# Optimization experiments

Measured on AMD Instinct MI355X. Metric: run time of the kernel, lower is better.

The kernel has to match this reference:

```python
import jax, jax.numpy as jnp
import numpy as np

TH = 0.1            # inference_th
PNUM = 20           # positive_num (also Pmax pad width for per-level top-k)
PLAM = 1.0          # positive_lambda
ANCHOR_SIZES = (64.0, 128.0)   # box_coder.anchor_sizes, one per FPN level
N, C = 2, 30
LEVELS = [(100, 136, 8, 64.0), (50, 68, 16, 128.0)]  # (H, W, stride, anchor_size)
NEG = -1e30


def make_anchors(H, W, stride, size):
    ys = (jnp.arange(H, dtype=jnp.float32) + 0.5) * stride
    xs = (jnp.arange(W, dtype=jnp.float32) + 0.5) * stride
    cy, cx = jnp.meshgrid(ys, xs, indexing='ij')
    cx, cy = cx.reshape(-1), cy.reshape(-1)
    h = size / 2.0
    return jnp.stack([cx - h, cy - h, cx + h, cy + h], axis=-1)  # [HW,4] x1y1x2y2


def setup_inputs() -> dict:
    key = jax.random.key(0)
    ks = iter(jax.random.split(key, 64))
    inp = {}
    for h in range(1, 5):
        for li, (H, W, _, _) in enumerate(LEVELS):
            suf = 'ab'[li]
            inp[f'cls{h}{suf}'] = jax.random.normal(next(ks), (N, C, H, W), jnp.float32)
            inp[f'reg{h}{suf}'] = jax.random.normal(next(ks), (N, C * 16, H, W), jnp.float32) * 0.1
    inp['anchors_a'] = make_anchors(*LEVELS[0])
    inp['anchors_b'] = make_anchors(*LEVELS[1])
    return inp


def _level(cls, reg, anchors):
    # permute_and_flatten (A=1) + sigmoid + threshold + dense keypoint decode
    n, c, H, W = cls.shape
    hw = H * W
    s = jax.nn.sigmoid(jnp.transpose(cls.reshape(n, c, hw), (0, 2, 1)))          # [N,HW,C]
    r = jnp.transpose(reg.reshape(n, c * 16, hw), (0, 2, 1)).reshape(n, hw, c, 16)
    x1, y1, x2, y2 = anchors[:, 0], anchors[:, 1], anchors[:, 2], anchors[:, 3]
    wa = (x2 - x1)[None, :, None, None]
    ha = (y2 - y1)[None, :, None, None]
    cxa = ((x1 + x2) * 0.5)[None, :, None, None]
    cya = ((y1 + y2) * 0.5)[None, :, None, None]
    kx = r[..., :8] * wa + cxa                                                    # 8 keypoint x's
    ky = r[..., 8:] * ha + cya                                                    # 8 keypoint y's
    dets = jnp.concatenate([kx, ky], axis=-1)                                     # [N,HW,C,16]
    mask = s > TH
    sm = jnp.where(mask, jnp.sqrt(s), NEG)   # original keeps sqrt(score) for candidates
    cnt = mask.sum(axis=1).astype(jnp.int32)                                      # [N,C]
    return sm, dets, cnt


def _head(levels):
    # pose_infer_ml per-label multi-level fusion, vectorized over all classes.
    a_sizes = jnp.asarray(ANCHOR_SIZES, jnp.float32)
    bests, sizes = [], []
    for sm, dets, cnt in levels:
        best = sm.max(axis=1)                                                     # [N,C]
        idx = sm.argmax(axis=1)                                                   # [N,C]
        nn, cc = idx.shape
        kb = jnp.take_along_axis(
            dets, jnp.broadcast_to(idx[:, None, :, None], (nn, 1, cc, 16)), axis=1)[:, 0]  # [N,C,16]
        kx, ky = kb[..., :8], kb[..., 8:]
        sz = jnp.maximum(kx.max(-1) - kx.min(-1), ky.max(-1) - ky.min(-1))
        bests.append(best)
        sizes.append(jnp.where(best > 0, sz, 0.0))
    best_l = jnp.stack(bests, axis=-1)                                            # [N,C,L]
    size_l = jnp.stack(sizes, axis=-1)                                            # [N,C,L]
    bi = jnp.argmax(best_l, axis=-1)
    box_size = jnp.take_along_axis(size_l, bi[..., None], axis=-1)[..., 0]        # [N,C]
    safe = jnp.where(box_size > 0, box_size, 1.0)
    dk = jnp.log2(safe[..., None] / a_sizes)                                      # [N,C,L]
    nk = jnp.exp(-PLAM * dk * dk)
    nk = PNUM * nk / nk.sum(-1, keepdims=True)
    nk = jnp.where(box_size[..., None] > 0, (nk + 0.5).astype(jnp.int32), 0)      # [N,C,L]
    outs = []
    for l, (sm, dets, cnt) in enumerate(levels):
        ts, ti = jax.lax.top_k(jnp.transpose(sm, (0, 2, 1)), PNUM)                # [N,C,P]
        dt = jnp.transpose(dets, (0, 2, 1, 3))                                    # [N,C,HW,16]
        td = jnp.take_along_axis(dt, ti[..., None], axis=2)                       # [N,C,P,16]
        pk = jnp.minimum(cnt, nk[..., l])                                         # [N,C]
        vm = (jnp.arange(PNUM)[None, None, :] < pk[..., None]) & (ts > 0)
        sc = jnp.where(vm, ts, 0.0)
        dd = jnp.where(vm[..., None], td, 0.0)
        outs.append(jnp.concatenate([sc[..., None], dd], axis=-1))               # [N,C,P,17]
    return jnp.stack(outs, axis=2)                                                # [N,C,L,P,17]


def reference(cls1a, reg1a, cls1b, reg1b, cls2a, reg2a, cls2b, reg2b,
              cls3a, reg3a, cls3b, reg3b, cls4a, reg4a, cls4b, reg4b,
              anchors_a, anchors_b):
    groups = [(cls1a, reg1a, cls1b, reg1b), (cls2a, reg2a, cls2b, reg2b),
              (cls3a, reg3a, cls3b, reg3b), (cls4a, reg4a, cls4b, reg4b)]
    heads = []
    for ca, ra, cb, rb in groups:
        lv = [_level(ca, ra, anchors_a), _level(cb, rb, anchors_b)]
        heads.append(_head(lv))
    return jnp.stack(heads, axis=1)  # [N, 4 heads, C, L, PNUM, 17] (score | 16 kpt coords)
```

## Files before the change

### kernel.cpp

```cpp
#include <hip/hip_runtime.h>
#include <hip/hip_bf16.h>
#include <math.h>

#define NB 2
#define NC 30
#define NH 4
#define HWA 13600
#define HWB 3400
#define PNUM 20
#define CAP2 256
#define LOGIT_TH -2.1972245773362196

struct Ptrs {
    const float* cls[8];
    const float* reg[8];
    const float* anc[2];
};

struct Sh {
    unsigned long long candU[CAP2];
    unsigned tw[4];
    int cw[4];
    int mcnt;
};

__device__ __forceinline__ unsigned f2key(float x) {
    unsigned u = __float_as_uint(x);
    return (u & 0x80000000u) ? ~u : (u | 0x80000000u);
}

template<int HW, int L>
__device__ __forceinline__ void topk_body(Sh& sh, const Ptrs& p, int bid,
                                          float* __restrict__ topv,
                                          int* __restrict__ topi,
                                          int* __restrict__ cnts) {
    constexpr int N4 = HW / 4;
    constexpr int NV = (N4 + 255) / 256;
    int c = bid % NC; int t = bid / NC;
    int n = t % NB;   int h = t / NB;
    int sid = ((h*2 + L)*NB + n)*NC + c;
    const float* base = p.cls[h*2 + L] + (size_t)(n*NC + c) * HW;
    int tid = threadIdx.x, lane = tid & 63, wv = tid >> 6;

    if (tid == 0) sh.mcnt = 0;

    float4 v[NV];
    #pragma unroll
    for (int i = 0; i < NV; ++i) {
        int f = tid + i * 256;
        if (f < N4) v[i] = ((const float4*)base)[f];
    }

    unsigned mk = 0u; int cnt = 0;
    #pragma unroll
    for (int i = 0; i < NV; ++i) {
        int f = tid + i * 256;
        if (f < N4) {
            float xs[4] = {v[i].x, v[i].y, v[i].z, v[i].w};
            #pragma unroll
            for (int j = 0; j < 4; ++j) {
                cnt += ((double)xs[j] > LOGIT_TH);
                unsigned k = f2key(xs[j]);
                mk = (k > mk) ? k : mk;
            }
        }
    }
    for (int off = 32; off; off >>= 1) cnt += __shfl_down(cnt, off);
    if (lane == 0) sh.cw[wv] = cnt;

    unsigned s = mk;
    #pragma unroll
    for (int k = 2; k <= 64; k <<= 1) {
        #pragma unroll
        for (int j = k >> 1; j > 0; j >>= 1) {
            unsigned o = __shfl_xor(s, j);
            bool up = ((lane & k) == 0);
            bool lower = ((lane & j) == 0);
            s = (up == lower) ? min(s, o) : max(s, o);
        }
    }
    unsigned t_w = __shfl(s, 64 - PNUM);
    if (lane == 0) sh.tw[wv] = t_w;
    __syncthreads();

    if (tid == 0) cnts[sid] = sh.cw[0] + sh.cw[1] + sh.cw[2] + sh.cw[3];
    unsigned tk = max(max(sh.tw[0], sh.tw[1]), max(sh.tw[2], sh.tw[3]));

    #pragma unroll
    for (int i = 0; i < NV; ++i) {
        int f = tid + i * 256;
        if (f < N4) {
            float xs[4] = {v[i].x, v[i].y, v[i].z, v[i].w};
            #pragma unroll
            for (int j = 0; j < 4; ++j) {
                unsigned key = f2key(xs[j]);
                if (key >= tk) {
                    int slot = atomicAdd(&sh.mcnt, 1);
                    if (slot < CAP2) {
                        int eidx = f * 4 + j;
                        sh.candU[slot] = ((unsigned long long)key << 32) |
                                         (unsigned)(~(unsigned)eidx);
                    }
                }
            }
        }
    }
    __syncthreads();

    int M = min(sh.mcnt, CAP2);
    if (tid < M) {
        unsigned long long mu = sh.candU[tid];
        int rank = 0;
        for (int m = 0; m < M; ++m) rank += (sh.candU[m] > mu);
        if (rank < PNUM) {
            unsigned key = (unsigned)(mu >> 32);
            unsigned u = (key & 0x80000000u) ? (key ^ 0x80000000u) : ~key;
            topv[sid * PNUM + rank] = __uint_as_float(u);
            topi[sid * PNUM + rank] = (int)~(unsigned)(mu & 0xFFFFFFFFu);
        }
    }
}

__global__ __launch_bounds__(256) void k_topk_all(Ptrs p, float* __restrict__ topv,
                                                  int* __restrict__ topi,
                                                  int* __restrict__ cnts) {
    __shared__ Sh sh;
    if (blockIdx.x < NH * NB * NC)
        topk_body<HWA, 0>(sh, p, blockIdx.x, topv, topi, cnts);
    else
        topk_body<HWB, 1>(sh, p, blockIdx.x - NH * NB * NC, topv, topi, cnts);
}

__global__ __launch_bounds__(64) void k_out(Ptrs p, const float* __restrict__ topv,
                                            const int* __restrict__ topi,
                                            const int* __restrict__ cnts,
                                            float* __restrict__ out) {
    __shared__ double sm[2 * PNUM];
    __shared__ int    idxs[2 * PNUM];
    __shared__ int    val[2 * PNUM];
    __shared__ double k16[2][16];
    __shared__ int    pk[2];

    int bid = blockIdx.x;
    int c = bid % NC; int t = bid / NC;
    int n = t % NB;   int h = t / NB;
    int tid = threadIdx.x;

    if (tid < 2 * PNUM) {
        int l = tid / PNUM, k = tid % PNUM;
        int sid = ((h*2 + l)*NB + n)*NC + c;
        float x = topv[sid * PNUM + k];
        int  ix = topi[sid * PNUM + k];
        idxs[tid] = ix;
        int v = ((double)x > LOGIT_TH);
        val[tid] = v;
        sm[tid] = v ? sqrt(1.0 / (1.0 + exp(-(double)x))) : -1e30;
    }
    __syncthreads();

    if (tid < 32) {
        int l = tid / 16, j = tid % 16;
        int hw = l ? HWB : HWA;
        int pos = idxs[l * PNUM];
        const float* reg = p.reg[h*2 + l];
        double r = (double)reg[((size_t)(n*NC*16 + c*16 + j)) * hw + pos];
        const float* anc = p.anc[l];
        double x1 = anc[pos*4+0], y1 = anc[pos*4+1], x2 = anc[pos*4+2], y2 = anc[pos*4+3];
        double kv;
        if (j < 8) kv = r * (x2 - x1) + (x1 + x2) * 0.5;
        else       kv = r * (y2 - y1) + (y1 + y2) * 0.5;
        k16[l][j] = kv;
    }
    __syncthreads();

    if (tid == 0) {
        double best[2], sz[2];
        for (int l = 0; l < 2; ++l) {
            best[l] = sm[l * PNUM];
            double kxmx = -1e300, kxmn = 1e300, kymx = -1e300, kymn = 1e300;
            for (int j = 0; j < 8; ++j) {
                double kx = k16[l][j], ky = k16[l][j + 8];
                kxmx = fmax(kxmx, kx); kxmn = fmin(kxmn, kx);
                kymx = fmax(kymx, ky); kymn = fmin(kymn, ky);
            }
            double s = fmax(kxmx - kxmn, kymx - kymn);
            sz[l] = (best[l] > 0.0) ? s : 0.0;
        }
        int bi = (best[0] >= best[1]) ? 0 : 1;
        double box = sz[bi];
        double safe = (box > 0.0) ? box : 1.0;
        double dk0 = log2(safe / 64.0), dk1 = log2(safe / 128.0);
        double e0 = exp(-dk0 * dk0), e1 = exp(-dk1 * dk1);
        double s = e0 + e1;
        int nk0 = (box > 0.0) ? (int)(20.0 * e0 / s + 0.5) : 0;
        int nk1 = (box > 0.0) ? (int)(20.0 * e1 / s + 0.5) : 0;
        int sid0 = ((h*2 + 0)*NB + n)*NC + c;
        int sid1 = ((h*2 + 1)*NB + n)*NC + c;
        pk[0] = min(cnts[sid0], nk0);
        pk[1] = min(cnts[sid1], nk1);
    }
    __syncthreads();

    if (tid < 2 * PNUM) {
        int l = tid / PNUM, k = tid % PNUM;
        int hw = l ? HWB : HWA;
        bool v = (k < pk[l]) && val[tid];
        size_t ob = ((((size_t)((n*NH + h)*NC + c)) * 2 + l) * PNUM + k) * 17;
        float* o = out + ob;
        if (!v) {
            #pragma unroll
            for (int e = 0; e < 17; ++e) o[e] = 0.f;
        } else {
            o[0] = (float)sm[tid];
            int pos = idxs[tid];
            const float* reg = p.reg[h*2 + l];
            const float* anc = p.anc[l];
            double x1 = anc[pos*4+0], y1 = anc[pos*4+1], x2 = anc[pos*4+2], y2 = anc[pos*4+3];
            double wa = x2 - x1, cxa = (x1 + x2) * 0.5;
            double ha = y2 - y1, cya = (y1 + y2) * 0.5;
            size_t rb = ((size_t)(n*NC*16 + c*16)) * hw + pos;
            #pragma unroll
            for (int j = 0; j < 8; ++j)
                o[1 + j] = (float)((double)reg[rb + (size_t)j * hw] * wa + cxa);
            #pragma unroll
            for (int j = 0; j < 8; ++j)
                o[9 + j] = (float)((double)reg[rb + (size_t)(j + 8) * hw] * ha + cya);
        }
    }
}

extern "C" void kernel_launch(void* const* d_in, const int* in_sizes, int n_in,
                              void* d_out, int out_size, void* d_ws, size_t ws_size,
                              hipStream_t stream) {
    Ptrs p;
    for (int h = 0; h < 4; ++h) {
        p.cls[h*2 + 0] = (const float*)d_in[h*4 + 0];
        p.reg[h*2 + 0] = (const float*)d_in[h*4 + 1];
        p.cls[h*2 + 1] = (const float*)d_in[h*4 + 2];
        p.reg[h*2 + 1] = (const float*)d_in[h*4 + 3];
    }
    p.anc[0] = (const float*)d_in[16];
    p.anc[1] = (const float*)d_in[17];

    const int NSER = NH * 2 * NB * NC;
    float* topv = (float*)d_ws;
    int*   topi = (int*)((char*)d_ws + (size_t)NSER * PNUM * 4);
    int*   cnts = (int*)((char*)d_ws + (size_t)NSER * PNUM * 8);

    k_topk_all<<<NSER, 256, 0, stream>>>(p, topv, topi, cnts);
    k_out<<<NH * NB * NC, 64, 0, stream>>>(p, topv, topi, cnts, (float*)d_out);
}
```

Before: 18.64 us.

## Fuse per-level top-k and output kernels into one block per head/class

New measurement: 21.29 us. +14.2%, slower.

```diff
diff --git a/kernel.cpp b/kernel.cpp
--- a/kernel.cpp
+++ b/kernel.cpp
@@ -1,5 +1,4 @@
 #include <hip/hip_runtime.h>
-#include <hip/hip_bf16.h>
 #include <math.h>
 
 #define NB 2
@@ -22,6 +21,13 @@
     unsigned tw[4];
     int cw[4];
     int mcnt;
+    float topv[2 * PNUM];
+    int   topi[2 * PNUM];
+    int   cnt[2];
+    double smv[2 * PNUM];
+    int    val[2 * PNUM];
+    double k16[2][16];
+    int    pk[2];
 };
 
 __device__ __forceinline__ unsigned f2key(float x) {
@@ -30,18 +36,12 @@
 }
 
 template<int HW, int L>
-__device__ __forceinline__ void topk_body(Sh& sh, const Ptrs& p, int bid,
-                                          float* __restrict__ topv,
-                                          int* __restrict__ topi,
-                                          int* __restrict__ cnts) {
+__device__ __forceinline__ void topk_body(Sh& sh, const float* __restrict__ base) {
     constexpr int N4 = HW / 4;
     constexpr int NV = (N4 + 255) / 256;
-    int c = bid % NC; int t = bid / NC;
-    int n = t % NB;   int h = t / NB;
-    int sid = ((h*2 + L)*NB + n)*NC + c;
-    const float* base = p.cls[h*2 + L] + (size_t)(n*NC + c) * HW;
     int tid = threadIdx.x, lane = tid & 63, wv = tid >> 6;
 
+    __syncthreads();
     if (tid == 0) sh.mcnt = 0;
 
     float4 v[NV];
@@ -83,7 +83,7 @@
     if (lane == 0) sh.tw[wv] = t_w;
     __syncthreads();
 
-    if (tid == 0) cnts[sid] = sh.cw[0] + sh.cw[1] + sh.cw[2] + sh.cw[3];
+    if (tid == 0) sh.cnt[L] = sh.cw[0] + sh.cw[1] + sh.cw[2] + sh.cw[3];
     unsigned tk = max(max(sh.tw[0], sh.tw[1]), max(sh.tw[2], sh.tw[3]));
 
     #pragma unroll
@@ -115,53 +115,37 @@
         if (rank < PNUM) {
             unsigned key = (unsigned)(mu >> 32);
             unsigned u = (key & 0x80000000u) ? (key ^ 0x80000000u) : ~key;
-            topv[sid * PNUM + rank] = __uint_as_float(u);
-            topi[sid * PNUM + rank] = (int)~(unsigned)(mu & 0xFFFFFFFFu);
-        }
-    }
-}
-
-__global__ __launch_bounds__(256) void k_topk_all(Ptrs p, float* __restrict__ topv,
-                                                  int* __restrict__ topi,
-                                                  int* __restrict__ cnts) {
+            sh.topv[L * PNUM + rank] = __uint_as_float(u);
+            sh.topi[L * PNUM + rank] = (int)~(unsigned)(mu & 0xFFFFFFFFu);
+        }
+    }
+}
+
+__global__ __launch_bounds__(256) void k_fused(Ptrs p, float* __restrict__ out) {
     __shared__ Sh sh;
-    if (blockIdx.x < NH * NB * NC)
-        topk_body<HWA, 0>(sh, p, blockIdx.x, topv, topi, cnts);
-    else
-        topk_body<HWB, 1>(sh, p, blockIdx.x - NH * NB * NC, topv, topi, cnts);
-}
-
-__global__ __launch_bounds__(64) void k_out(Ptrs p, const float* __restrict__ topv,
-                                            const int* __restrict__ topi,
-                                            const int* __restrict__ cnts,
-                                            float* __restrict__ out) {
-    __shared__ double sm[2 * PNUM];
-    __shared__ int    idxs[2 * PNUM];
-    __shared__ int    val[2 * PNUM];
-    __shared__ double k16[2][16];
-    __shared__ int    pk[2];
-
     int bid = blockIdx.x;
     int c = bid % NC; int t = bid / NC;
     int n = t % NB;   int h = t / NB;
     int tid = threadIdx.x;
 
+    if (tid < 2 * PNUM) { sh.topv[tid] = -1e30f; sh.topi[tid] = 0; }
+
+    topk_body<HWA, 0>(sh, p.cls[h*2 + 0] + (size_t)(n*NC + c) * HWA);
+    topk_body<HWB, 1>(sh, p.cls[h*2 + 1] + (size_t)(n*NC + c) * HWB);
+    __syncthreads();
+
     if (tid < 2 * PNUM) {
-        int l = tid / PNUM, k = tid % PNUM;
-        int sid = ((h*2 + l)*NB + n)*NC + c;
-        float x = topv[sid * PNUM + k];
-        int  ix = topi[sid * PNUM + k];
-        idxs[tid] = ix;
+        float x = sh.topv[tid];
         int v = ((double)x > LOGIT_TH);
-        val[tid] = v;
-        sm[tid] = v ? sqrt(1.0 / (1.0 + exp(-(double)x))) : -1e30;
+        sh.val[tid] = v;
+        sh.smv[tid] = v ? sqrt(1.0 / (1.0 + exp(-(double)x))) : -1e30;
     }
     __syncthreads();
 
     if (tid < 32) {
         int l = tid / 16, j = tid % 16;
         int hw = l ? HWB : HWA;
-        int pos = idxs[l * PNUM];
+        int pos = sh.topi[l * PNUM];
         const float* reg = p.reg[h*2 + l];
         double r = (double)reg[((size_t)(n*NC*16 + c*16 + j)) * hw + pos];
         const float* anc = p.anc[l];
@@ -169,17 +153,17 @@
         double kv;
         if (j < 8) kv = r * (x2 - x1) + (x1 + x2) * 0.5;
         else       kv = r * (y2 - y1) + (y1 + y2) * 0.5;
-        k16[l][j] = kv;
+        sh.k16[l][j] = kv;
     }
     __syncthreads();
 
     if (tid == 0) {
         double best[2], sz[2];
         for (int l = 0; l < 2; ++l) {
-            best[l] = sm[l * PNUM];
+            best[l] = sh.smv[l * PNUM];
             double kxmx = -1e300, kxmn = 1e300, kymx = -1e300, kymn = 1e300;
             for (int j = 0; j < 8; ++j) {
-                double kx = k16[l][j], ky = k16[l][j + 8];
+                double kx = sh.k16[l][j], ky = sh.k16[l][j + 8];
                 kxmx = fmax(kxmx, kx); kxmn = fmin(kxmn, kx);
                 kymx = fmax(kymx, ky); kymn = fmin(kymn, ky);
             }
@@ -194,25 +178,23 @@
         double s = e0 + e1;
         int nk0 = (box > 0.0) ? (int)(20.0 * e0 / s + 0.5) : 0;
         int nk1 = (box > 0.0) ? (int)(20.0 * e1 / s + 0.5) : 0;
-        int sid0 = ((h*2 + 0)*NB + n)*NC + c;
-        int sid1 = ((h*2 + 1)*NB + n)*NC + c;
-        pk[0] = min(cnts[sid0], nk0);
-        pk[1] = min(cnts[sid1], nk1);
+        sh.pk[0] = min(sh.cnt[0], nk0);
+        sh.pk[1] = min(sh.cnt[1], nk1);
     }
     __syncthreads();
 
     if (tid < 2 * PNUM) {
         int l = tid / PNUM, k = tid % PNUM;
         int hw = l ? HWB : HWA;
-        bool v = (k < pk[l]) && val[tid];
+        bool v = (k < sh.pk[l]) && sh.val[tid];
         size_t ob = ((((size_t)((n*NH + h)*NC + c)) * 2 + l) * PNUM + k) * 17;
         float* o = out + ob;
         if (!v) {
             #pragma unroll
             for (int e = 0; e < 17; ++e) o[e] = 0.f;
         } else {
-            o[0] = (float)sm[tid];
-            int pos = idxs[tid];
+            o[0] = (float)sh.smv[tid];
+            int pos = sh.topi[tid];
             const float* reg = p.reg[h*2 + l];
             const float* anc = p.anc[l];
             double x1 = anc[pos*4+0], y1 = anc[pos*4+1], x2 = anc[pos*4+2], y2 = anc[pos*4+3];
@@ -242,11 +224,5 @@
     p.anc[0] = (const float*)d_in[16];
     p.anc[1] = (const float*)d_in[17];
 
-    const int NSER = NH * 2 * NB * NC;
-    float* topv = (float*)d_ws;
-    int*   topi = (int*)((char*)d_ws + (size_t)NSER * PNUM * 4);
-    int*   cnts = (int*)((char*)d_ws + (size_t)NSER * PNUM * 8);
-
-    k_topk_all<<<NSER, 256, 0, stream>>>(p, topv, topi, cnts);
-    k_out<<<NH * NB * NC, 64, 0, stream>>>(p, topv, topi, cnts, (float*)d_out);
-}
+    k_fused<<<NH * NB * NC, 256, 0, stream>>>(p, (float*)d_out);
+}
```

## Split level-A top-k across four chunk blocks and merge partial top-k in output kernel

Applied to the files above, without the earlier changes.

After: 20.62 us. 1.11x slower.

```diff
diff --git a/kernel.cpp b/kernel.cpp
--- a/kernel.cpp
+++ b/kernel.cpp
@@ -1,5 +1,4 @@
 #include <hip/hip_runtime.h>
-#include <hip/hip_bf16.h>
 #include <math.h>
 
 #define NB 2
@@ -9,6 +8,11 @@
 #define HWB 3400
 #define PNUM 20
 #define CAP2 256
+#define NPAIR (NH * NB * NC)
+#define NCH 4
+#define N4C 850
+#define NSUBA (NPAIR * NCH)
+#define NSUB  (NSUBA + NPAIR)
 #define LOGIT_TH -2.1972245773362196
 
 struct Ptrs {
@@ -29,20 +33,38 @@
     return (u & 0x80000000u) ? ~u : (u | 0x80000000u);
 }
 
-template<int HW, int L>
-__device__ __forceinline__ void topk_body(Sh& sh, const Ptrs& p, int bid,
-                                          float* __restrict__ topv,
-                                          int* __restrict__ topi,
-                                          int* __restrict__ cnts) {
-    constexpr int N4 = HW / 4;
+__global__ __launch_bounds__(256) void k_topk_all(Ptrs p, float* __restrict__ topv,
+                                                  int* __restrict__ topi,
+                                                  int* __restrict__ cnts) {
+    __shared__ Sh sh;
+    int bid = blockIdx.x;
+    const float* base;
+    int elemOff;
+    {
+        int pair, hslot;
+        if (bid < NSUBA) {
+            pair = bid >> 2; int ch = bid & 3;
+            int c = pair % NC; int t = pair / NC;
+            int n = t % NB;   int h = t / NB;
+            hslot = h*2 + 0;
+            base = p.cls[hslot] + (size_t)(n*NC + c) * HWA + (size_t)ch * (N4C * 4);
+            elemOff = ch * (N4C * 4);
+        } else {
+            pair = bid - NSUBA;
+            int c = pair % NC; int t = pair / NC;
+            int n = t % NB;   int h = t / NB;
+            hslot = h*2 + 1;
+            base = p.cls[hslot] + (size_t)(n*NC + c) * HWB;
+            elemOff = 0;
+        }
+    }
+    int sid2 = bid;
+    int tid = threadIdx.x, lane = tid & 63, wv = tid >> 6;
+
+    if (tid == 0) sh.mcnt = 0;
+
+    constexpr int N4 = N4C;
     constexpr int NV = (N4 + 255) / 256;
-    int c = bid % NC; int t = bid / NC;
-    int n = t % NB;   int h = t / NB;
-    int sid = ((h*2 + L)*NB + n)*NC + c;
-    const float* base = p.cls[h*2 + L] + (size_t)(n*NC + c) * HW;
-    int tid = threadIdx.x, lane = tid & 63, wv = tid >> 6;
-
-    if (tid == 0) sh.mcnt = 0;
 
     float4 v[NV];
     #pragma unroll
@@ -83,7 +105,7 @@
     if (lane == 0) sh.tw[wv] = t_w;
     __syncthreads();
 
-    if (tid == 0) cnts[sid] = sh.cw[0] + sh.cw[1] + sh.cw[2] + sh.cw[3];
+    if (tid == 0) cnts[sid2] = sh.cw[0] + sh.cw[1] + sh.cw[2] + sh.cw[3];
     unsigned tk = max(max(sh.tw[0], sh.tw[1]), max(sh.tw[2], sh.tw[3]));
 
     #pragma unroll
@@ -97,7 +119,7 @@
                 if (key >= tk) {
                     int slot = atomicAdd(&sh.mcnt, 1);
                     if (slot < CAP2) {
-                        int eidx = f * 4 + j;
+                        int eidx = elemOff + f * 4 + j;
                         sh.candU[slot] = ((unsigned long long)key << 32) |
                                          (unsigned)(~(unsigned)eidx);
                     }
@@ -115,46 +137,57 @@
         if (rank < PNUM) {
             unsigned key = (unsigned)(mu >> 32);
             unsigned u = (key & 0x80000000u) ? (key ^ 0x80000000u) : ~key;
-            topv[sid * PNUM + rank] = __uint_as_float(u);
-            topi[sid * PNUM + rank] = (int)~(unsigned)(mu & 0xFFFFFFFFu);
-        }
-    }
-}
-
-__global__ __launch_bounds__(256) void k_topk_all(Ptrs p, float* __restrict__ topv,
-                                                  int* __restrict__ topi,
-                                                  int* __restrict__ cnts) {
-    __shared__ Sh sh;
-    if (blockIdx.x < NH * NB * NC)
-        topk_body<HWA, 0>(sh, p, blockIdx.x, topv, topi, cnts);
-    else
-        topk_body<HWB, 1>(sh, p, blockIdx.x - NH * NB * NC, topv, topi, cnts);
+            topv[sid2 * PNUM + rank] = __uint_as_float(u);
+            topi[sid2 * PNUM + rank] = (int)~(unsigned)(mu & 0xFFFFFFFFu);
+        }
+    }
 }
 
 __global__ __launch_bounds__(64) void k_out(Ptrs p, const float* __restrict__ topv,
                                             const int* __restrict__ topi,
                                             const int* __restrict__ cnts,
                                             float* __restrict__ out) {
+    __shared__ float  tvA[NCH * PNUM];
+    __shared__ int    idxA[NCH * PNUM];
+    __shared__ unsigned long long candM[NCH * PNUM];
+    __shared__ float  tv2[2 * PNUM];
+    __shared__ int    idxs[2 * PNUM];
     __shared__ double sm[2 * PNUM];
-    __shared__ int    idxs[2 * PNUM];
     __shared__ int    val[2 * PNUM];
     __shared__ double k16[2][16];
     __shared__ int    pk[2];
-
-    int bid = blockIdx.x;
-    int c = bid % NC; int t = bid / NC;
+    __shared__ int    cnt2[2];
+
+    int pair = blockIdx.x;
+    int c = pair % NC; int t = pair / NC;
     int n = t % NB;   int h = t / NB;
     int tid = threadIdx.x;
 
-    if (tid < 2 * PNUM) {
-        int l = tid / PNUM, k = tid % PNUM;
-        int sid = ((h*2 + l)*NB + n)*NC + c;
-        float x = topv[sid * PNUM + k];
-        int  ix = topi[sid * PNUM + k];
-        idxs[tid] = ix;
-        int v = ((double)x > LOGIT_TH);
-        val[tid] = v;
-        sm[tid] = v ? sqrt(1.0 / (1.0 + exp(-(double)x))) : -1e30;
+    for (int e = tid; e < NCH * PNUM; e += 64) {
+        int ch = e / PNUM, k = e % PNUM;
+        int sid2 = pair * NCH + ch;
+        float x = topv[sid2 * PNUM + k];
+        int  ix = topi[sid2 * PNUM + k];
+        tvA[e] = x; idxA[e] = ix;
+        candM[e] = ((unsigned long long)f2key(x) << 32) | (unsigned)(~(unsigned)ix);
+    }
+    if (tid < PNUM) {
+        int sid2 = NSUBA + pair;
+        tv2[PNUM + tid]  = topv[sid2 * PNUM + tid];
+        idxs[PNUM + tid] = topi[sid2 * PNUM + tid];
+    }
+    if (tid == 0) {
+        cnt2[0] = cnts[pair*NCH + 0] + cnts[pair*NCH + 1]
+                + cnts[pair*NCH + 2] + cnts[pair*NCH + 3];
+        cnt2[1] = cnts[NSUBA + pair];
+    }
+    __syncthreads();
+
+    for (int e = tid; e < NCH * PNUM; e += 64) {
+        unsigned long long mu = candM[e];
+        int rank = 0;
+        for (int m = 0; m < NCH * PNUM; ++m) rank += (candM[m] > mu);
+        if (rank < PNUM) { tv2[rank] = tvA[e]; idxs[rank] = idxA[e]; }
     }
     __syncthreads();
 
@@ -171,6 +204,12 @@
         else       kv = r * (y2 - y1) + (y1 + y2) * 0.5;
         k16[l][j] = kv;
     }
+    if (tid < 2 * PNUM) {
+        float x = tv2[tid];
+        int v = ((double)x > LOGIT_TH);
+        val[tid] = v;
+        sm[tid] = v ? sqrt(1.0 / (1.0 + exp(-(double)x))) : -1e30;
+    }
     __syncthreads();
 
     if (tid == 0) {
@@ -194,10 +233,8 @@
         double s = e0 + e1;
         int nk0 = (box > 0.0) ? (int)(20.0 * e0 / s + 0.5) : 0;
         int nk1 = (box > 0.0) ? (int)(20.0 * e1 / s + 0.5) : 0;
-        int sid0 = ((h*2 + 0)*NB + n)*NC + c;
-        int sid1 = ((h*2 + 1)*NB + n)*NC + c;
-        pk[0] = min(cnts[sid0], nk0);
-        pk[1] = min(cnts[sid1], nk1);
+        pk[0] = min(cnt2[0], nk0);
+        pk[1] = min(cnt2[1], nk1);
     }
     __syncthreads();
 
@@ -242,11 +279,10 @@
     p.anc[0] = (const float*)d_in[16];
     p.anc[1] = (const float*)d_in[17];
 
-    const int NSER = NH * 2 * NB * NC;
     float* topv = (float*)d_ws;
-    int*   topi = (int*)((char*)d_ws + (size_t)NSER * PNUM * 4);
-    int*   cnts = (int*)((char*)d_ws + (size_t)NSER * PNUM * 8);
-
-    k_topk_all<<<NSER, 256, 0, stream>>>(p, topv, topi, cnts);
-    k_out<<<NH * NB * NC, 64, 0, stream>>>(p, topv, topi, cnts, (float*)d_out);
-}
+    int*   topi = (int*)((char*)d_ws + (size_t)NSUB * PNUM * 4);
+    int*   cnts = (int*)((char*)d_ws + (size_t)NSUB * PNUM * 8);
+
+    k_topk_all<<<NSUB, 256, 0, stream>>>(p, topv, topi, cnts);
+    k_out<<<NPAIR, 64, 0, stream>>>(p, topv, topi, cnts, (float*)d_out);
+}
```
